# Optimization experiments

Measured on AMD Instinct MI355X. Metric: run time of the kernel, lower is better.

## Reference

```python
import jax, jax.numpy as jnp
import numpy as np
from jax import lax

B, W, H, C = 32, 512, 512, 3
PSF = 32


def setup_inputs() -> dict:
    key = jax.random.key(0)
    k1, k2, k3 = jax.random.split(key, 3)
    observed_images = jax.random.normal(k1, (B, W, H, C), dtype=jnp.float32)
    # trainable vars of the keras model (estimated_image would be initialized to
    # mean(observed) on the first call; we treat it as a free parameter)
    estimated_image = jax.random.normal(k2, (W, H, C), dtype=jnp.float32)
    point_spread_functions = jax.random.normal(k3, (B, PSF, PSF, 1, C), dtype=jnp.float32) * 0.05
    return {
        "observed_images": observed_images,
        "estimated_image": estimated_image,
        "point_spread_functions": point_spread_functions,
    }


def _per_example_conv(img_nhwc, psf_hwio):
    # img_nhwc: [1, W, H, C]; psf_hwio: [k, k, 1, C] -> grouped (depthwise) conv,
    # feature_group_count = C, matching tf.nn.conv2d's grouped-conv semantics.
    out = lax.conv_general_dilated(
        img_nhwc, psf_hwio,
        window_strides=(1, 1), padding="SAME",
        dimension_numbers=("NHWC", "HWIO", "NHWC"),
        feature_group_count=img_nhwc.shape[-1],
    )
    return out[0]  # [W, H, C]


def reference(observed_images, estimated_image, point_spread_functions):
    img = estimated_image[None]  # [1, W, H, C], shared across batch
    # vmap over the per-example PSF kernels replaces the python loop of B conv2d calls
    predicted = jax.vmap(lambda psf: _per_example_conv(img, psf))(point_spread_functions)
    # predicted: [B, W, H, C]
    loss = jnp.mean((observed_images - predicted) ** 2)
    return predicted, loss
```

## Files before the change

### kernel.cpp

```cpp
#include <hip/hip_runtime.h>
#include <hip/hip_bf16.h>

#define BATCH 32
#define WDIM 512
#define HDIM 512
#define CDIM 3
#define KPSF 32
#define NPRED (BATCH*WDIM*HDIM*CDIM)

#define TW 88
#define TH 63
#define TE (TW*TH)
#define TALL (TW*TH*CDIM)

typedef __bf16 bf16x8 __attribute__((ext_vector_type(8)));
typedef float floatx16 __attribute__((ext_vector_type(16)));

__global__ __launch_bounds__(64) void pack_psf(const float* __restrict__ psf,
                                               __bf16* __restrict__ dst,
                                               float* __restrict__ loss) {
    if (blockIdx.x == 0 && threadIdx.x == 0) *loss = 0.f;
    int idx = blockIdx.x;
    int h = idx & 1;
    int j = (idx >> 1) & 31;
    int c = idx >> 6;
    int lane = threadIdx.x;
    int b = lane & 31;
    int q = lane >> 5;
    bf16x8 v;
#pragma unroll
    for (int t = 0; t < 8; ++t) {
        int i = 16*h + 8*q + t;
        v[t] = (__bf16)psf[((size_t)(b*KPSF + i)*KPSF + j)*CDIM + c];
    }
    *(bf16x8*)(dst + (size_t)(idx*64 + lane)*8) = v;
}

__global__ __launch_bounds__(192, 2) void conv_mfma(
    const float* __restrict__ obs,
    const float* __restrict__ img,
    const __bf16* __restrict__ psfA,
    float* __restrict__ out)
{
    __shared__ __align__(16) unsigned char smem[CDIM*TE*2];
    __bf16 (*sImg)[TE] = (__bf16 (*)[TE])smem;
    float* sOut = (float*)smem;

    const int tid  = threadIdx.x;
    const int lane = tid & 63;
    const int c    = tid >> 6;
    const int n    = lane & 31;
    const int q    = lane >> 5;

    const int bx = blockIdx.x;
    const int r  = bx & 7;
    const int g  = (bx >> 3) & 7;
    const int yt = bx >> 6;
    const int x0 = g*64 + r;
    const int ytile = yt*32;

    const bool interior = (x0 >= 15) && (x0 <= WDIM - 73) &&
                          (ytile >= 15) && (ytile <= HDIM - 48);
    if (interior) {
        const float* ibase = img + ((size_t)(x0-15)*HDIM + (ytile-15))*CDIM;
#pragma unroll 4
        for (int e = tid; e < TALL; e += 192) {
            int xl = e / (TH*CDIM);
            int rr = e - xl*(TH*CDIM);
            int yl = rr / 3;
            int cc = rr - yl*3;
            float v = ibase[(size_t)xl*(HDIM*CDIM) + rr];
            sImg[cc][yl*TW + xl] = (__bf16)v;
        }
    } else {
#pragma unroll 4
        for (int e = tid; e < TALL; e += 192) {
            int xl = e / (TH*CDIM);
            int rr = e - xl*(TH*CDIM);
            int yl = rr / 3;
            int cc = rr - yl*3;
            int xg = x0 + xl - 15;
            int yg = ytile + yl - 15;
            float v = 0.f;
            if ((unsigned)xg < WDIM && (unsigned)yg < HDIM)
                v = img[((size_t)xg*HDIM + yg)*CDIM + cc];
            sImg[cc][yl*TW + xl] = (__bf16)v;
        }
    }
    __syncthreads();

    floatx16 acc[8] = {};
    const __bf16* pA = psfA + (size_t)c*(KPSF*2*64*8) + (size_t)lane*8;
    const __bf16* sI = (const __bf16*)&sImg[c][q*8];

    bf16x8 A0 = *(const bf16x8*)(pA);
    bf16x8 A1 = *(const bf16x8*)(pA + 512);
#pragma unroll 4
    for (int j = 0; j < 32; ++j) {
        bf16x8 cA0 = A0, cA1 = A1;
        if (j < 31) {
            A0 = *(const bf16x8*)(pA + (size_t)(j+1)*1024);
            A1 = *(const bf16x8*)(pA + (size_t)(j+1)*1024 + 512);
        }
        const __bf16* rowp = sI + (n + j)*TW;
        bf16x8 C[10];
#pragma unroll
        for (int rr = 0; rr < 10; ++rr)
            C[rr] = *(const bf16x8*)(rowp + rr*8);
#pragma unroll
        for (int s = 0; s < 8; ++s) {
            acc[s] = __builtin_amdgcn_mfma_f32_32x32x16_bf16(cA0, C[s],   acc[s], 0, 0, 0);
            acc[s] = __builtin_amdgcn_mfma_f32_32x32x16_bf16(cA1, C[s+2], acc[s], 0, 0, 0);
        }
    }

    float ls = 0.f;
#pragma unroll 1
    for (int s = 0; s < 8; ++s) {
        __syncthreads();
#pragma unroll
        for (int rr = 0; rr < 16; ++rr) {
            int b = (rr & 3) + 8*(rr >> 2) + 4*q;
            sOut[(b*32 + n)*3 + c] = acc[s][rr];
        }
        __syncthreads();
        const int x = x0 + 8*s;
#pragma unroll
        for (int k = 0; k < 4; ++k) {
            int f = tid + 192*k;
            int fb = f / 24;
            int rem = (f - fb*24) * 4;
            size_t o = (((size_t)fb*WDIM + x)*HDIM + ytile)*CDIM + rem;
            float4 p = *(const float4*)&sOut[4*f];
            float4 ob = *(const float4*)&obs[o];
            *(float4*)&out[o] = p;
            float d0 = ob.x - p.x, d1 = ob.y - p.y;
            float d2 = ob.z - p.z, d3 = ob.w - p.w;
            ls += d0*d0 + d1*d1 + d2*d2 + d3*d3;
        }
    }

#pragma unroll
    for (int m = 32; m >= 1; m >>= 1) ls += __shfl_xor(ls, m, 64);
    if (lane == 0) atomicAdd(out + NPRED, ls * (1.0f/(float)NPRED));
}

extern "C" void kernel_launch(void* const* d_in, const int* in_sizes, int n_in,
                              void* d_out, int out_size, void* d_ws, size_t ws_size,
                              hipStream_t stream) {
    const float* obs = (const float*)d_in[0];
    const float* img = (const float*)d_in[1];
    const float* psf = (const float*)d_in[2];
    float* out = (float*)d_out;
    __bf16* psfA = (__bf16*)d_ws;

    pack_psf<<<192, 64, 0, stream>>>(psf, psfA, out + NPRED);
    conv_mfma<<<1024, 192, 0, stream>>>(obs, img, psfA, out);
}
```

Measured before the change: 269.8 us.

## Split conv block work across two waves per channel and prefetch observations

Doubles the block to 384 threads, so each channel's MFMA work is split between two waves that each handle half of the output columns, with four accumulators per wave instead of eight. This roughly halves per-wave register pressure and accumulator work and raises the number of waves per CU. The epilogue now loads the observed-image tiles one step ahead, overlapping global reads with the LDS transposition and output stores. The risk is that each wave reloads the shared PSF A-operands and duplicates some LDS row reads, and the larger blocks may limit how many blocks fit per CU.

```diff
diff --git a/kernel.cpp b/kernel.cpp
--- a/kernel.cpp
+++ b/kernel.cpp
@@ -36,7 +36,7 @@
     *(bf16x8*)(dst + (size_t)(idx*64 + lane)*8) = v;
 }
 
-__global__ __launch_bounds__(192, 2) void conv_mfma(
+__global__ __launch_bounds__(384, 3) void conv_mfma(
     const float* __restrict__ obs,
     const float* __restrict__ img,
     const __bf16* __restrict__ psfA,
@@ -48,7 +48,9 @@
 
     const int tid  = threadIdx.x;
     const int lane = tid & 63;
-    const int c    = tid >> 6;
+    const int w    = tid >> 6;
+    const int c    = w >> 1;
+    const int sh   = w & 1;
     const int n    = lane & 31;
     const int q    = lane >> 5;
 
@@ -64,7 +66,7 @@
     if (interior) {
         const float* ibase = img + ((size_t)(x0-15)*HDIM + (ytile-15))*CDIM;
 #pragma unroll 4
-        for (int e = tid; e < TALL; e += 192) {
+        for (int e = tid; e < TALL; e += 384) {
             int xl = e / (TH*CDIM);
             int rr = e - xl*(TH*CDIM);
             int yl = rr / 3;
@@ -74,7 +76,7 @@
         }
     } else {
 #pragma unroll 4
-        for (int e = tid; e < TALL; e += 192) {
+        for (int e = tid; e < TALL; e += 384) {
             int xl = e / (TH*CDIM);
             int rr = e - xl*(TH*CDIM);
             int yl = rr / 3;
@@ -89,9 +91,9 @@
     }
     __syncthreads();
 
-    floatx16 acc[8] = {};
+    floatx16 acc[4] = {};
     const __bf16* pA = psfA + (size_t)c*(KPSF*2*64*8) + (size_t)lane*8;
-    const __bf16* sI = (const __bf16*)&sImg[c][q*8];
+    const __bf16* sI = (const __bf16*)&sImg[c][q*8 + sh*32];
 
     bf16x8 A0 = *(const bf16x8*)(pA);
     bf16x8 A1 = *(const bf16x8*)(pA + 512);
@@ -103,41 +105,53 @@
             A1 = *(const bf16x8*)(pA + (size_t)(j+1)*1024 + 512);
         }
         const __bf16* rowp = sI + (n + j)*TW;
-        bf16x8 C[10];
+        bf16x8 C[6];
 #pragma unroll
-        for (int rr = 0; rr < 10; ++rr)
+        for (int rr = 0; rr < 6; ++rr)
             C[rr] = *(const bf16x8*)(rowp + rr*8);
 #pragma unroll
-        for (int s = 0; s < 8; ++s) {
-            acc[s] = __builtin_amdgcn_mfma_f32_32x32x16_bf16(cA0, C[s],   acc[s], 0, 0, 0);
-            acc[s] = __builtin_amdgcn_mfma_f32_32x32x16_bf16(cA1, C[s+2], acc[s], 0, 0, 0);
+        for (int ss = 0; ss < 4; ++ss) {
+            acc[ss] = __builtin_amdgcn_mfma_f32_32x32x16_bf16(cA0, C[ss],   acc[ss], 0, 0, 0);
+            acc[ss] = __builtin_amdgcn_mfma_f32_32x32x16_bf16(cA1, C[ss+2], acc[ss], 0, 0, 0);
         }
     }
 
     float ls = 0.f;
+    size_t base0, base1;
+    {
+        int f0 = tid,       fb0 = f0 / 24, rem0 = (f0 - fb0*24) * 4;
+        int f1 = tid + 384, fb1 = f1 / 24, rem1 = (f1 - fb1*24) * 4;
+        base0 = (((size_t)fb0*WDIM + x0)*HDIM + ytile)*CDIM + rem0;
+        base1 = (((size_t)fb1*WDIM + x0)*HDIM + ytile)*CDIM + rem1;
+    }
+    float4 ob0 = *(const float4*)&obs[base0];
+    float4 ob1 = *(const float4*)&obs[base1];
+
 #pragma unroll 1
     for (int s = 0; s < 8; ++s) {
         __syncthreads();
+        if (sh == (s >> 2)) {
+            const int ss = s & 3;
 #pragma unroll
-        for (int rr = 0; rr < 16; ++rr) {
-            int b = (rr & 3) + 8*(rr >> 2) + 4*q;
-            sOut[(b*32 + n)*3 + c] = acc[s][rr];
+            for (int rr = 0; rr < 16; ++rr) {
+                int b = (rr & 3) + 8*(rr >> 2) + 4*q;
+                sOut[(b*32 + n)*3 + c] = acc[ss][rr];
+            }
         }
         __syncthreads();
-        const int x = x0 + 8*s;
-#pragma unroll
-        for (int k = 0; k < 4; ++k) {
-            int f = tid + 192*k;
-            int fb = f / 24;
-            int rem = (f - fb*24) * 4;
-            size_t o = (((size_t)fb*WDIM + x)*HDIM + ytile)*CDIM + rem;
-            float4 p = *(const float4*)&sOut[4*f];
-            float4 ob = *(const float4*)&obs[o];
-            *(float4*)&out[o] = p;
-            float d0 = ob.x - p.x, d1 = ob.y - p.y;
-            float d2 = ob.z - p.z, d3 = ob.w - p.w;
-            ls += d0*d0 + d1*d1 + d2*d2 + d3*d3;
+        float4 c0 = ob0, c1 = ob1;
+        if (s < 7) {
+            ob0 = *(const float4*)&obs[base0 + (size_t)(s+1)*8*HDIM*CDIM];
+            ob1 = *(const float4*)&obs[base1 + (size_t)(s+1)*8*HDIM*CDIM];
         }
+        float4 p0 = *(const float4*)&sOut[4*tid];
+        float4 p1 = *(const float4*)&sOut[4*(tid + 384)];
+        *(float4*)&out[base0 + (size_t)s*8*HDIM*CDIM] = p0;
+        *(float4*)&out[base1 + (size_t)s*8*HDIM*CDIM] = p1;
+        float d0 = c0.x - p0.x, d1 = c0.y - p0.y, d2 = c0.z - p0.z, d3 = c0.w - p0.w;
+        float e0 = c1.x - p1.x, e1 = c1.y - p1.y, e2 = c1.z - p1.z, e3 = c1.w - p1.w;
+        ls += d0*d0 + d1*d1 + d2*d2 + d3*d3;
+        ls += e0*e0 + e1*e1 + e2*e2 + e3*e3;
     }
 
 #pragma unroll
@@ -155,5 +169,5 @@
     __bf16* psfA = (__bf16*)d_ws;
 
     pack_psf<<<192, 64, 0, stream>>>(psf, psfA, out + NPRED);
-    conv_mfma<<<1024, 192, 0, stream>>>(obs, img, psfA, out);
+    conv_mfma<<<1024, 384, 0, stream>>>(obs, img, psfA, out);
 }
```

After: 306.4 us. +13.6%, slower.

## Vectorize interior image staging and prefetch observed tiles with nontemporal epilogue I/O

Applied to the files above, without the earlier changes.

Interior tile staging now reads the image with float4 loads per row and scatters the values into per-channel bf16 shared arrays, replacing scalar loads with divisions. The epilogue precomputes output offsets and double-buffers the observed-image loads two slices ahead with nontemporal loads, so global latency overlaps the shared-memory transposes. Output stores become nontemporal, and __syncthreads is replaced by an inline-asm lgkmcnt wait plus s_barrier that does not wait on outstanding vector memory. This costs extra registers (32 floats of prefetch buffers) and may cut occupancy.

```diff
diff --git a/kernel.cpp b/kernel.cpp
--- a/kernel.cpp
+++ b/kernel.cpp
@@ -15,6 +15,11 @@
 
 typedef __bf16 bf16x8 __attribute__((ext_vector_type(8)));
 typedef float floatx16 __attribute__((ext_vector_type(16)));
+typedef float fx4 __attribute__((ext_vector_type(4)));
+
+__device__ __forceinline__ void barrier_lgkm() {
+    __asm__ volatile("s_waitcnt lgkmcnt(0)\n\ts_barrier" ::: "memory");
+}
 
 __global__ __launch_bounds__(64) void pack_psf(const float* __restrict__ psf,
                                                __bf16* __restrict__ dst,
@@ -53,24 +58,33 @@
     const int q    = lane >> 5;
 
     const int bx = blockIdx.x;
-    const int r  = bx & 7;
+    const int r8 = bx & 7;
     const int g  = (bx >> 3) & 7;
     const int yt = bx >> 6;
-    const int x0 = g*64 + r;
+    const int x0 = g*64 + r8;
     const int ytile = yt*32;
 
     const bool interior = (x0 >= 15) && (x0 <= WDIM - 73) &&
                           (ytile >= 15) && (ytile <= HDIM - 48);
     if (interior) {
-        const float* ibase = img + ((size_t)(x0-15)*HDIM + (ytile-15))*CDIM;
-#pragma unroll 4
-        for (int e = tid; e < TALL; e += 192) {
-            int xl = e / (TH*CDIM);
-            int rr = e - xl*(TH*CDIM);
-            int yl = rr / 3;
-            int cc = rr - yl*3;
-            float v = ibase[(size_t)xl*(HDIM*CDIM) + rr];
-            sImg[cc][yl*TW + xl] = (__bf16)v;
+        const int col0 = (ytile - 15)*3;
+        const int p2 = col0 & 3;
+        const float* gb = img + (size_t)(x0 - 15)*(HDIM*CDIM) + (col0 - p2);
+#pragma unroll 2
+        for (int f = tid; f < 88*48; f += 192) {
+            int r = f / 48;
+            int v = f - r*48;
+            fx4 val = *(const fx4*)(gb + (size_t)r*(HDIM*CDIM) + 4*v);
+            int d = 4*v - p2;
+#pragma unroll
+            for (int u = 0; u < 4; ++u) {
+                int dd = d + u;
+                if (dd >= 0 && dd < 189) {
+                    int yl = (dd*171) >> 9;
+                    int cc = dd - 3*yl;
+                    sImg[cc][yl*TW + r] = (__bf16)val[u];
+                }
+            }
         }
     } else {
 #pragma unroll 4
@@ -115,28 +129,46 @@
     }
 
     float ls = 0.f;
+    size_t base[4];
+#pragma unroll
+    for (int k = 0; k < 4; ++k) {
+        int f = tid + 192*k;
+        int fb = f / 24;
+        int rem = (f - fb*24) * 4;
+        base[k] = (((size_t)fb*WDIM + x0)*HDIM + ytile)*CDIM + rem;
+    }
+    fx4 obA[4], obB[4];
+#pragma unroll
+    for (int k = 0; k < 4; ++k)
+        obA[k] = __builtin_nontemporal_load((const fx4*)&obs[base[k]]);
+#pragma unroll
+    for (int k = 0; k < 4; ++k)
+        obB[k] = __builtin_nontemporal_load((const fx4*)&obs[base[k] + 8*HDIM*CDIM]);
+
 #pragma unroll 1
     for (int s = 0; s < 8; ++s) {
-        __syncthreads();
+        barrier_lgkm();
 #pragma unroll
         for (int rr = 0; rr < 16; ++rr) {
             int b = (rr & 3) + 8*(rr >> 2) + 4*q;
             sOut[(b*32 + n)*3 + c] = acc[s][rr];
         }
-        __syncthreads();
-        const int x = x0 + 8*s;
+        barrier_lgkm();
+        fx4 cur[4];
+#pragma unroll
+        for (int k = 0; k < 4; ++k) { cur[k] = obA[k]; obA[k] = obB[k]; }
+        if (s < 6) {
+#pragma unroll
+            for (int k = 0; k < 4; ++k)
+                obB[k] = __builtin_nontemporal_load(
+                    (const fx4*)&obs[base[k] + (size_t)(s+2)*8*HDIM*CDIM]);
+        }
 #pragma unroll
         for (int k = 0; k < 4; ++k) {
-            int f = tid + 192*k;
-            int fb = f / 24;
-            int rem = (f - fb*24) * 4;
-            size_t o = (((size_t)fb*WDIM + x)*HDIM + ytile)*CDIM + rem;
-            float4 p = *(const float4*)&sOut[4*f];
-            float4 ob = *(const float4*)&obs[o];
-            *(float4*)&out[o] = p;
-            float d0 = ob.x - p.x, d1 = ob.y - p.y;
-            float d2 = ob.z - p.z, d3 = ob.w - p.w;
-            ls += d0*d0 + d1*d1 + d2*d2 + d3*d3;
+            fx4 p = *(const fx4*)&sOut[4*(tid + 192*k)];
+            __builtin_nontemporal_store(p, (fx4*)&out[base[k] + (size_t)s*8*HDIM*CDIM]);
+            fx4 d = cur[k] - p;
+            ls += d[0]*d[0] + d[1]*d[1] + d[2]*d[2] + d[3]*d[3];
         }
     }
 
```

New measurement: 263.1 us. 1.03x faster.
